# Kernel tuning notes

Measured on AMD Instinct MI355X. Metric: run time of the kernel, lower is better.

## Reference

```python
import jax, jax.numpy as jnp
import numpy as np
import math

T = 2048; HID = 2048; H = 16; KV = 8; G = H // KV; D = 128
GH = 128; BS = 64; NB = T // BS
EPS = 1e-6; RATIO = 0.2; SCALE = 1.0 / math.sqrt(D)


def _rope_tables(length, dim, theta=1000000.0):
    inv = 1.0 / (theta ** (np.arange(0, dim, 2, dtype=np.float32) / dim))
    f = np.outer(np.arange(length, dtype=np.float32), inv)
    emb = np.concatenate([f, f], axis=-1)
    return jnp.asarray(np.cos(emb)), jnp.asarray(np.sin(emb))


def _rot_half(x):
    d = x.shape[-1] // 2
    return jnp.concatenate([-x[..., d:], x[..., :d]], axis=-1)


def _apply_rope(x, cos, sin):
    # x: [T, nH, D], cos/sin: [T, D] broadcast over head dim
    return x * cos[:, None, :] + _rot_half(x) * sin[:, None, :]


def _rmsnorm(x, w, eps=EPS):
    xf = x.astype(jnp.float32)
    v = jnp.mean(xf * xf, axis=-1, keepdims=True)
    return (w * (xf * jax.lax.rsqrt(v + eps))).astype(x.dtype)


def setup_inputs() -> dict:
    key = jax.random.key(0)
    ks = jax.random.split(key, 8)
    s = 0.02
    hidden_states = jax.random.normal(ks[0], (T, HID), jnp.float32)
    Wq = jax.random.normal(ks[1], (HID, H * D), jnp.float32) * s
    Wk = jax.random.normal(ks[2], (HID, KV * D), jnp.float32) * s
    Wv = jax.random.normal(ks[3], (HID, KV * D), jnp.float32) * s
    Wo = jax.random.normal(ks[4], (H * D, HID), jnp.float32) * s
    q_norm_w = jnp.ones((D,), jnp.float32)
    k_norm_w = jnp.ones((D,), jnp.float32)
    gate_wq = jax.random.normal(ks[5], (D, GH), jnp.float32) * s
    gate_wk = jax.random.normal(ks[6], (D, GH), jnp.float32) * s
    cos, sin = _rope_tables(T, D)
    cos_gq, sin_gq = _rope_tables(T, GH)
    cos_blk, sin_blk = _rope_tables(NB, GH)
    # causal block mask: query t may attend to key block j iff j <= t // BS
    block_attention_mask = (jnp.arange(T)[:, None] // BS) >= jnp.arange(NB)[None, :]
    return dict(hidden_states=hidden_states, Wq=Wq, Wk=Wk, Wv=Wv, Wo=Wo,
                q_norm_w=q_norm_w, k_norm_w=k_norm_w, gate_wq=gate_wq, gate_wk=gate_wk,
                cos=cos, sin=sin, cos_gq=cos_gq, sin_gq=sin_gq,
                cos_blk=cos_blk, sin_blk=sin_blk,
                block_attention_mask=block_attention_mask)


def reference(hidden_states, Wq, Wk, Wv, Wo, q_norm_w, k_norm_w, gate_wq, gate_wk,
              cos, sin, cos_gq, sin_gq, cos_blk, sin_blk, block_attention_mask):
    q = (hidden_states @ Wq).reshape(T, H, D)
    k = (hidden_states @ Wk).reshape(T, KV, D)
    v = (hidden_states @ Wv).reshape(T, KV, D)
    q = _rmsnorm(q, q_norm_w)
    k = _rmsnorm(k, k_norm_w)

    # ---- gate network on un-roped q/k: q-head avg-pool to KV heads, k avg-pool per block ----
    q_pool = q.reshape(T, KV, G, D).mean(axis=2)            # [T, KV, D]
    gq = _apply_rope(q_pool @ gate_wq, cos_gq, sin_gq)      # [T, KV, GH]
    k_blk = k.reshape(NB, BS, KV, D).mean(axis=1)           # [NB, KV, D]
    gk = _apply_rope(k_blk @ gate_wk, cos_blk, sin_blk)     # [NB, KV, GH]
    gate_scores = jnp.einsum('tkg,nkg->ktn', gq, gk) / math.sqrt(GH)  # [KV, T, NB]
    predict_mask = jnp.where(block_attention_mask[None], gate_scores, -1e9)

    # ---- main attention (RoPE + GQA causal softmax attention) ----
    qr = _apply_rope(q, cos, sin)
    kr = _apply_rope(k, cos, sin)
    kr_rep = jnp.repeat(kr, G, axis=1)                      # [T, H, D]
    v_rep = jnp.repeat(v, G, axis=1)
    logits = jnp.einsum('thd,shd->hts', qr, kr_rep) * SCALE  # [H, T, T]
    causal = jnp.tril(jnp.ones((T, T), bool))
    logits = jnp.where(causal[None], logits, -jnp.inf)
    probs = jax.nn.softmax(logits, axis=-1)
    attn_output = jnp.einsum('hts,shd->thd', probs, v_rep).reshape(T, H * D) @ Wo

    # ---- pooled ground-truth block mask: attention mass per key block ----
    pooled = probs.reshape(H, T, NB, BS).sum(axis=-1)        # [H, T, NB]
    gt = pooled.reshape(KV, G, T, NB).max(axis=1)            # max_pool3d over head groups -> [KV,T,NB]
    gt = jnp.where(block_attention_mask[None], gt, 0.0)
    gt = gt / (gt.sum(axis=-1, keepdims=True) + 1e-9)

    # ---- KLDiv gate loss on the tail slice (bsz = 1) ----
    start = int(T * RATIO)
    tgt = gt[:, start:, :]                                   # [KV, L, NB]
    logp = jax.nn.log_softmax(predict_mask[:, start:, :], axis=-1)
    safe_t = jnp.where(tgt > 0, tgt, 1.0)
    kl = jnp.where(tgt > 0, tgt * (jnp.log(safe_t) - logp), 0.0)
    gate_loss = kl.reshape(KV, -1).mean(axis=-1).sum()       # KLDivLoss(reduction='mean') per kv head, summed, /bsz(=1)
    return attn_output, gate_loss
```

## Files before the change

kernel.cpp:

```cpp
#include <hip/hip_runtime.h>

#define T_ 2048
#define HID_ 2048
#define H_ 16
#define KV_ 8
#define G_ 2
#define D_ 128
#define GH_ 128
#define BS_ 64
#define NB_ 32
#define START_ 409
#define TG0_ 384
#define SCALE_ 0.08838834764831845f
#define MFIX_ 8.0f

typedef __attribute__((ext_vector_type(8))) short short8_t;
typedef __attribute__((ext_vector_type(4))) float float4_t;
typedef __attribute__((ext_vector_type(8))) unsigned short ushort8_t;
typedef __attribute__((ext_vector_type(4))) unsigned short ushort4_t;

__device__ __forceinline__ float wave_sum(float v) {
#pragma unroll
  for (int o = 32; o > 0; o >>= 1) v += __shfl_xor(v, o, 64);
  return v;
}
__device__ __forceinline__ unsigned short f2bf(float x) {
  unsigned int u = __float_as_uint(x);
  unsigned int r = (u + 0x7fffu + ((u >> 16) & 1u)) >> 16;
  return (unsigned short)r;
}

__device__ __forceinline__ void gload16(const void* g, void* l) {
  __builtin_amdgcn_global_load_lds((const __attribute__((address_space(1))) unsigned int*)g,
                                   (__attribute__((address_space(3))) unsigned int*)l, 16, 0, 0);
}

__device__ __forceinline__ void castT_dev(const float* __restrict__ in,
                                          unsigned short* __restrict__ out, int K, int N,
                                          int ldin, int bx, int by,
                                          unsigned short (*tile)[72], int tid) {
  int k0 = by * 64, n0 = bx * 64;
  int tx = tid & 63, ty4 = tid >> 6;
#pragma unroll
  for (int i = 0; i < 16; ++i) {
    int ky = ty4 * 16 + i;
    tile[tx][ky] = f2bf(in[(size_t)(k0 + ky) * ldin + n0 + tx]);
  }
  __syncthreads();
#pragma unroll
  for (int i = 0; i < 16; ++i) {
    int ny = ty4 * 16 + i;
    out[(size_t)(n0 + ny) * K + k0 + tx] = tile[ny][tx];
  }
}

__global__ __launch_bounds__(256) void prep_cast(const float* __restrict__ hs,
                                                 const float* __restrict__ Wq,
                                                 const float* __restrict__ Wk,
                                                 const float* __restrict__ Wv,
                                                 const float* __restrict__ Wo,
                                                 const float* __restrict__ gwq,
                                                 const float* __restrict__ gwk,
                                                 unsigned short* __restrict__ hsb,
                                                 unsigned short* __restrict__ WqkvT,
                                                 unsigned short* __restrict__ WoT,
                                                 unsigned short* __restrict__ gwqT,
                                                 unsigned short* __restrict__ gwkT) {
  __shared__ unsigned short tile[64][72];
  int id = blockIdx.x, tid = threadIdx.x;
  if (id < 4096) {
    int i = id * 256 + tid;
    float4 v = ((const float4*)hs)[i];
    ushort4_t o = {f2bf(v.x), f2bf(v.y), f2bf(v.z), f2bf(v.w)};
    *(ushort4_t*)(hsb + (size_t)i * 4) = o;
  } else if (id < 5120) {
    int t = id - 4096;
    castT_dev(Wq, WqkvT, 2048, 2048, 2048, t & 31, t >> 5, tile, tid);
  } else if (id < 5632) {
    int t = id - 5120;
    castT_dev(Wk, WqkvT + (size_t)2048 * 2048, 2048, 1024, 1024, t & 15, t >> 4, tile, tid);
  } else if (id < 6144) {
    int t = id - 5632;
    castT_dev(Wv, WqkvT + (size_t)3072 * 2048, 2048, 1024, 1024, t & 15, t >> 4, tile, tid);
  } else if (id < 7168) {
    int t = id - 6144;
    castT_dev(Wo, WoT, 2048, 2048, 2048, t & 31, t >> 5, tile, tid);
  } else if (id < 7172) {
    int t = id - 7168;
    castT_dev(gwq, gwqT, 128, 128, 128, t & 1, t >> 1, tile, tid);
  } else {
    int t = id - 7172;
    castT_dev(gwk, gwkT, 128, 128, 128, t & 1, t >> 1, tile, tid);
  }
}

__device__ __forceinline__ void gemm_body(const unsigned short* __restrict__ A,
                                          const unsigned short* __restrict__ Bt,
                                          float* __restrict__ C,
                                          int M, int N, int K, int ldc, int bx, int by,
                                          unsigned short* As, unsigned short* Bs) {
  int tid = threadIdx.x;
  int wid = tid >> 6, lane = tid & 63;
  int quad = lane >> 4, l16 = lane & 15;
  int wm = wid & 1, wn = wid >> 1;
  int m0 = by * 128, n0 = bx * 128;
  const unsigned short* gA[4];
  const unsigned short* gB[4];
#pragma unroll
  for (int it = 0; it < 4; ++it) {
    int line = wid * 32 + it * 8 + (lane >> 3);
    int chunk = (lane & 7) ^ (line & 7);
    gA[it] = A + (size_t)(m0 + line) * K + chunk * 8;
    gB[it] = Bt + (size_t)(n0 + line) * K + chunk * 8;
  }
  float4_t acc[4][4];
#pragma unroll
  for (int i = 0; i < 4; ++i)
#pragma unroll
    for (int j = 0; j < 4; ++j) acc[i][j] = (float4_t){0.f, 0.f, 0.f, 0.f};
  int nk = K >> 6;
#pragma unroll
  for (int it = 0; it < 4; ++it) {
    gload16(gA[it], As + (wid * 32 + it * 8) * 64);
    gload16(gB[it], Bs + (wid * 32 + it * 8) * 64);
  }
  for (int t = 0; t < nk; ++t) {
    __syncthreads();
    if (t + 1 < nk) {
      int bo = ((t + 1) & 1) * 8192;
#pragma unroll
      for (int it = 0; it < 4; ++it) {
        gload16(gA[it] + (t + 1) * 64, As + bo + (wid * 32 + it * 8) * 64);
        gload16(gB[it] + (t + 1) * 64, Bs + bo + (wid * 32 + it * 8) * 64);
      }
    }
    const unsigned short* Asc = As + (t & 1) * 8192;
    const unsigned short* Bsc = Bs + (t & 1) * 8192;
    short8_t a[2][4], b[2][4];
#pragma unroll
    for (int ks = 0; ks < 2; ++ks) {
      int sw = ((ks * 4 + quad) ^ (l16 & 7)) * 8;
#pragma unroll
      for (int i = 0; i < 4; ++i) {
        a[ks][i] = *(const short8_t*)&Asc[(wm * 64 + i * 16 + l16) * 64 + sw];
        b[ks][i] = *(const short8_t*)&Bsc[(wn * 64 + i * 16 + l16) * 64 + sw];
      }
    }
#pragma unroll
    for (int ks = 0; ks < 2; ++ks)
#pragma unroll
      for (int i = 0; i < 4; ++i)
#pragma unroll
        for (int j = 0; j < 4; ++j)
          acc[i][j] = __builtin_amdgcn_mfma_f32_16x16x32_bf16(a[ks][i], b[ks][j], acc[i][j], 0, 0, 0);
  }
#pragma unroll
  for (int i = 0; i < 4; ++i)
#pragma unroll
    for (int j = 0; j < 4; ++j)
#pragma unroll
      for (int reg = 0; reg < 4; ++reg)
        C[(size_t)(m0 + wm * 64 + i * 16 + quad * 4 + reg) * ldc + n0 + wn * 64 + j * 16 + l16] =
            acc[i][j][reg];
}

__global__ __launch_bounds__(256) void gemm_bf16_v3(const unsigned short* __restrict__ A,
                                                    const unsigned short* __restrict__ Bt,
                                                    float* __restrict__ C,
                                                    int M, int N, int K, int ldc) {
  __shared__ unsigned short As[2 * 128 * 64];
  __shared__ unsigned short Bs[2 * 128 * 64];
  int lin = blockIdx.y * gridDim.x + blockIdx.x;
  int nwg = gridDim.x * gridDim.y;
  int q = nwg >> 3;
  int v = (lin & 7) * q + (lin >> 3);
  int bx = v % gridDim.x, by = v / gridDim.x;
  gemm_body(A, Bt, C, M, N, K, ldc, bx, by, As, Bs);
}

__global__ __launch_bounds__(128) void norm_rope_fused(const float* __restrict__ qkvf,
                                                       const float* __restrict__ qw,
                                                       const float* __restrict__ kw,
                                                       const float* __restrict__ cosT,
                                                       const float* __restrict__ sinT,
                                                       unsigned short* __restrict__ qbf,
                                                       unsigned short* __restrict__ qpool_bf,
                                                       unsigned short* __restrict__ kbf,
                                                       float* __restrict__ knorm) {
  int t = blockIdx.x, d = threadIdx.x;
  int kv = blockIdx.y;
  float cv = cosT[t * D_ + d], sv = sinT[t * D_ + d];
  {
    size_t i0 = (size_t)t * 4096 + (kv * G_) * D_ + d;
    float x0 = qkvf[i0], x1 = qkvf[i0 + D_];
    __shared__ float sred[2][2];
    float s0 = wave_sum(x0 * x0), s1 = wave_sum(x1 * x1);
    if ((d & 63) == 0) { sred[0][d >> 6] = s0; sred[1][d >> 6] = s1; }
    __syncthreads();
    float wv = qw[d];
    float n0 = x0 * rsqrtf((sred[0][0] + sred[0][1]) * (1.f / D_) + 1e-6f) * wv;
    float n1 = x1 * rsqrtf((sred[1][0] + sred[1][1]) * (1.f / D_) + 1e-6f) * wv;
    if (t >= TG0_) qpool_bf[((size_t)(t - TG0_) * KV_ + kv) * D_ + d] = f2bf(0.5f * (n0 + n1));
    __shared__ float sh[2][D_];
    sh[0][d] = n0; sh[1][d] = n1;
    __syncthreads();
    float r0 = (d < 64) ? -sh[0][d + 64] : sh[0][d - 64];
    float r1 = (d < 64) ? -sh[1][d + 64] : sh[1][d - 64];
    qbf[((size_t)(t * H_) + kv * G_) * D_ + d] = f2bf(n0 * cv + r0 * sv);
    qbf[((size_t)(t * H_) + kv * G_ + 1) * D_ + d] = f2bf(n1 * cv + r1 * sv);
  }
  __syncthreads();
  {
    float x = qkvf[(size_t)t * 4096 + 2048 + kv * D_ + d];
    __shared__ float sredk[2];
    float s0 = wave_sum(x * x);
    if ((d & 63) == 0) sredk[d >> 6] = s0;
    __syncthreads();
    float nk = x * rsqrtf((sredk[0] + sredk[1]) * (1.f / D_) + 1e-6f) * kw[d];
    knorm[(size_t)(t * KV_ + kv) * D_ + d] = nk;
    __shared__ float shk[D_];
    shk[d] = nk;
    __syncthreads();
    float rot = (d < 64) ? -shk[d + 64] : shk[d - 64];
    kbf[(size_t)(t * KV_ + kv) * D_ + d] = f2bf(nk * cv + rot * sv);
  }
}

__global__ __launch_bounds__(256) void castT_kblk(const float* __restrict__ qkvf,
                                                  unsigned short* __restrict__ vt,
                                                  const float* __restrict__ knorm,
                                                  unsigned short* __restrict__ kblk_bf) {
  __shared__ unsigned short tile[64][72];
  int id = blockIdx.x, tid = threadIdx.x;
  if (id < 512) {
    castT_dev(qkvf + 3072, vt, T_, 1024, 4096, id & 15, id >> 4, tile, tid);
  } else {
    int task = (id - 512) * 2 + (tid >> 7);
    int n = task >> 3, kv = task & 7, d = tid & 127;
    float s = 0.f;
    for (int i = 0; i < BS_; ++i) s += knorm[((size_t)(n * BS_ + i) * KV_ + kv) * D_ + d];
    kblk_bf[(size_t)(n * KV_ + kv) * D_ + d] = f2bf(s * (1.f / BS_));
  }
}

__global__ __launch_bounds__(128) void rope_g_fused(float* __restrict__ gq, float* __restrict__ gk,
                                                    const float* __restrict__ cosG,
                                                    const float* __restrict__ sinG,
                                                    const float* __restrict__ cosB,
                                                    const float* __restrict__ sinB) {
  int r = blockIdx.x, kvh = blockIdx.y, d = threadIdx.x;
  float* x;
  size_t base;
  float c_, s_;
  if (r < NB_) {
    x = gk;
    base = (size_t)(r * KV_ + kvh) * GH_;
    c_ = cosB[r * GH_ + d]; s_ = sinB[r * GH_ + d];
  } else {
    int rr = r - NB_;
    x = gq;
    base = (size_t)(rr * KV_ + kvh) * GH_;
    c_ = cosG[(size_t)(TG0_ + rr) * GH_ + d]; s_ = sinG[(size_t)(TG0_ + rr) * GH_ + d];
  }
  __shared__ float sh[GH_];
  sh[d] = x[base + d];
  __syncthreads();
  float rot = (d < 64) ? -sh[d + 64] : sh[d - 64];
  x[base + d] = sh[d] * c_ + rot * s_;
}

__global__ __launch_bounds__(256, 2) void attn_gates(const unsigned short* __restrict__ qbf,
                                                     const unsigned short* __restrict__ kbf,
                                                     const unsigned short* __restrict__ vt,
                                                     float* __restrict__ pooled,
                                                     float* __restrict__ o_acc,
                                                     float* __restrict__ l_acc,
                                                     const unsigned short* __restrict__ Aq,
                                                     const unsigned short* __restrict__ Bq,
                                                     float* __restrict__ Cq,
                                                     const unsigned short* __restrict__ Ak,
                                                     const unsigned short* __restrict__ Bk,
                                                     float* __restrict__ Ck) {
  __shared__ unsigned short Ks[2][64 * 128];
  __shared__ unsigned short Vs[2][128 * 64];
  __shared__ unsigned short Ps[8][16 * 64];
  int kv = blockIdx.x;
  int yy = blockIdx.y;
  if (yy >= 64) {
    int g2 = kv + ((yy - 64) << 3);
    unsigned short* As = &Ks[0][0];
    unsigned short* Bs = &Vs[0][0];
    if (g2 < 104)      gemm_body(Aq, Bq, Cq, 13312, 128, 128, 128, 0, g2, As, Bs);
    else if (g2 < 106) gemm_body(Ak, Bk, Ck, 256, 128, 128, 128, 0, g2 - 104, As, Bs);
    return;
  }
  int tile, c_lo, c_hi;
  if (yy < 32) { tile = yy;      c_lo = 0;                c_hi = (tile + 2) >> 1; }
  else         { tile = 63 - yy; c_lo = (tile + 2) >> 1;  c_hi = tile + 1; }
  int t0 = tile * 64;
  int tid = threadIdx.x;
  int wid = tid >> 6, lane = tid & 63;
  int quad = lane >> 4, l16 = lane & 15;

  const unsigned short* kbase[4];
  const unsigned short* vbase[4];
#pragma unroll
  for (int it = 0; it < 4; ++it) {
    int seg = wid * 4 + it;
    int krow = seg * 4 + (lane >> 4);
    int kchk = lane & 15;
    kbase[it] = kbf + ((size_t)krow * KV_ + kv) * D_ + ((kchk ^ (krow & 7)) << 3);
    int vrow = seg * 8 + (lane >> 3);
    int vchk = lane & 7;
    vbase[it] = vt + (size_t)(kv * 128 + vrow) * T_ + ((vchk ^ (vrow & 7)) << 3);
  }

  int tq = t0 + wid * 16 + l16;
  short8_t qf[2][4];
#pragma unroll
  for (int hh = 0; hh < 2; ++hh)
#pragma unroll
    for (int kb = 0; kb < 4; ++kb)
      qf[hh][kb] = *(const short8_t*)&qbf[((size_t)tq * H_ + kv * G_ + hh) * D_ + kb * 32 + quad * 8];

  const short one_bf = (short)0x3F80;
  short8_t ones = {one_bf, one_bf, one_bf, one_bf, one_bf, one_bf, one_bf, one_bf};

  int tbase = t0 + wid * 16 + quad * 4;
  float l_[2][4] = {};
  float pacc[2][2][4] = {};
  float4_t o[2][8];
#pragma unroll
  for (int hh = 0; hh < 2; ++hh)
#pragma unroll
    for (int j = 0; j < 8; ++j) o[hh][j] = (float4_t){0.f, 0.f, 0.f, 0.f};

#pragma unroll
  for (int it = 0; it < 4; ++it) {
    gload16(kbase[it] + (size_t)c_lo * 65536, &Ks[c_lo & 1][(wid * 4 + it) * 512]);
    gload16(vbase[it] + c_lo * 64, &Vs[c_lo & 1][(wid * 4 + it) * 512]);
  }
  for (int c = c_lo; c < c_hi; ++c) {
    __syncthreads();
    if (c + 1 < c_hi) {
      int b = (c + 1) & 1;
#pragma unroll
      for (int it = 0; it < 4; ++it) {
        gload16(kbase[it] + (size_t)(c + 1) * 65536, &Ks[b][(wid * 4 + it) * 512]);
        gload16(vbase[it] + (c + 1) * 64, &Vs[b][(wid * 4 + it) * 512]);
      }
    }
    const unsigned short* Ksc = Ks[c & 1];
    const unsigned short* Vsc = Vs[c & 1];
    int half = c >> 4, cl = c & 15;

    float4_t s[2][4];
#pragma unroll
    for (int j = 0; j < 4; ++j) {
      float4_t a0 = (float4_t){0.f, 0.f, 0.f, 0.f};
      float4_t a1 = (float4_t){0.f, 0.f, 0.f, 0.f};
#pragma unroll
      for (int kb = 0; kb < 4; ++kb) {
        short8_t kf = *(const short8_t*)&Ksc[(j * 16 + l16) * 128 + (((kb * 4 + quad) ^ (l16 & 7)) << 3)];
        a0 = __builtin_amdgcn_mfma_f32_16x16x32_bf16(qf[0][kb], kf, a0, 0, 0, 0);
        a1 = __builtin_amdgcn_mfma_f32_16x16x32_bf16(qf[1][kb], kf, a1, 0, 0, 0);
      }
      s[0][j] = a0;
      s[1][j] = a1;
    }
#pragma unroll
    for (int hh = 0; hh < 2; ++hh) {
      if (c == tile) {
#pragma unroll
        for (int reg = 0; reg < 4; ++reg) {
          int trow = tbase + reg;
#pragma unroll
          for (int j = 0; j < 4; ++j) {
            float p = __expf(s[hh][j][reg] * SCALE_ - MFIX_);
            s[hh][j][reg] = (c * 64 + j * 16 + l16 <= trow) ? p : 0.f;
          }
        }
      } else {
#pragma unroll
        for (int j = 0; j < 4; ++j)
#pragma unroll
          for (int reg = 0; reg < 4; ++reg)
            s[hh][j][reg] = __expf(s[hh][j][reg] * SCALE_ - MFIX_);
      }
#pragma unroll
      for (int j = 0; j < 4; ++j)
#pragma unroll
        for (int reg = 0; reg < 4; ++reg) {
          int r = quad * 4 + reg;
          Ps[wid * 2 + hh][r * 64 + ((j * 16 + l16) ^ ((r & 7) << 3))] = f2bf(s[hh][j][reg]);
        }
    }
    float4_t pool[2] = {(float4_t){0.f, 0.f, 0.f, 0.f}, (float4_t){0.f, 0.f, 0.f, 0.f}};
#pragma unroll
    for (int ks = 0; ks < 2; ++ks) {
      int psw = l16 * 64 + (((ks * 4 + quad) ^ (l16 & 7)) << 3);
      short8_t pf0 = *(const short8_t*)&Ps[wid * 2 + 0][psw];
      short8_t pf1 = *(const short8_t*)&Ps[wid * 2 + 1][psw];
      pool[0] = __builtin_amdgcn_mfma_f32_16x16x32_bf16(pf0, ones, pool[0], 0, 0, 0);
      pool[1] = __builtin_amdgcn_mfma_f32_16x16x32_bf16(pf1, ones, pool[1], 0, 0, 0);
#pragma unroll
      for (int jt = 0; jt < 8; ++jt) {
        short8_t vf = *(const short8_t*)&Vsc[(jt * 16 + l16) * 64 + (((ks * 4 + quad) ^ (l16 & 7)) << 3)];
        o[0][jt] = __builtin_amdgcn_mfma_f32_16x16x32_bf16(pf0, vf, o[0][jt], 0, 0, 0);
        o[1][jt] = __builtin_amdgcn_mfma_f32_16x16x32_bf16(pf1, vf, o[1][jt], 0, 0, 0);
      }
    }
#pragma unroll
    for (int hh = 0; hh < 2; ++hh)
#pragma unroll
      for (int reg = 0; reg < 4; ++reg) {
        l_[hh][reg] += pool[hh][reg];
        if (l16 == cl) pacc[hh][half][reg] = pool[hh][reg];
      }
  }
#pragma unroll
  for (int hh = 0; hh < 2; ++hh) {
    int h = kv * G_ + hh;
#pragma unroll
    for (int reg = 0; reg < 4; ++reg) {
      int trow = tbase + reg;
      if (l16 >= c_lo && l16 < c_hi)
        pooled[((size_t)h * T_ + trow) * NB_ + l16] = pacc[hh][0][reg];
      if (16 + l16 >= c_lo && 16 + l16 < c_hi)
        pooled[((size_t)h * T_ + trow) * NB_ + 16 + l16] = pacc[hh][1][reg];
    }
#pragma unroll
    for (int jt = 0; jt < 8; ++jt)
#pragma unroll
      for (int reg = 0; reg < 4; ++reg)
        atomicAdd(&o_acc[(((size_t)h * T_) + tbase + reg) * D_ + jt * 16 + l16], o[hh][jt][reg]);
    if (l16 == 0) {
#pragma unroll
      for (int reg = 0; reg < 4; ++reg)
        atomicAdd(&l_acc[(size_t)h * T_ + tbase + reg], l_[hh][reg]);
    }
  }
}

__device__ __forceinline__ void gate_loss_body(const float* __restrict__ gq,
                                               const float* __restrict__ gk,
                                               const float* __restrict__ pooled,
                                               const float* __restrict__ l_acc,
                                               float* __restrict__ klsum,
                                               int kv, int yblk, float4* gks4) {
  int tid = threadIdx.x;
#pragma unroll
  for (int p = 0; p < 4; ++p) {
    int f = p * 256 + tid;
    int n = f >> 5, d4 = f & 31;
    gks4[n * 32 + (d4 ^ (n & 7))] =
        *(const float4*)(gk + ((size_t)n * KV_ + kv) * GH_ + d4 * 4);
  }
  __syncthreads();
  int sub = tid >> 5;
  int n = tid & 31;
  int tloc = yblk * 8 + sub;
  bool act = tloc < (T_ - START_);
  int t = START_ + (act ? tloc : 0);
  const float4* a = (const float4*)(gq + ((size_t)(t - TG0_) * KV_ + kv) * GH_);
  float dot = 0.f;
#pragma unroll
  for (int d4 = 0; d4 < 32; ++d4) {
    float4 av = a[d4];
    float4 bv = gks4[n * 32 + (d4 ^ (n & 7))];
    dot += av.x * bv.x + av.y * bv.y + av.z * bv.z + av.w * bv.w;
  }
  bool valid = (t / BS_) >= n;
  float score = valid ? dot * SCALE_ : -1e9f;
  float M = score;
#pragma unroll
  for (int o = 16; o > 0; o >>= 1) M = fmaxf(M, __shfl_xor(M, o, 64));
  float e = __expf(score - M);
  float Z = e;
#pragma unroll
  for (int o = 16; o > 0; o >>= 1) Z += __shfl_xor(Z, o, 64);
  float logZ = M + logf(Z);
  float g = 0.f;
  if (valid) {
    float rl0 = 1.f / l_acc[(size_t)(kv * G_) * T_ + t];
    float rl1 = 1.f / l_acc[(size_t)(kv * G_ + 1) * T_ + t];
    float p0 = pooled[((size_t)(kv * G_) * T_ + t) * NB_ + n] * rl0;
    float p1 = pooled[((size_t)(kv * G_ + 1) * T_ + t) * NB_ + n] * rl1;
    g = fmaxf(p0, p1);
  }
  float gs = g;
#pragma unroll
  for (int o = 16; o > 0; o >>= 1) gs += __shfl_xor(gs, o, 64);
  float tgt = g / (gs + 1e-9f);
  float kl = (tgt > 0.f) ? tgt * (logf(tgt) - (score - logZ)) : 0.f;
  float ks = kl;
#pragma unroll
  for (int o = 16; o > 0; o >>= 1) ks += __shfl_xor(ks, o, 64);
  if (n == 0 && act) klsum[kv * (T_ - START_) + tloc] = ks;
}

__global__ __launch_bounds__(256) void combine_gate(const float* __restrict__ o_acc,
                                                    const float* __restrict__ l_acc,
                                                    unsigned short* __restrict__ attnb,
                                                    const float* __restrict__ gq,
                                                    const float* __restrict__ gk,
                                                    const float* __restrict__ pooled,
                                                    float* __restrict__ klsum) {
  __shared__ float4 gks4[1024];
  int id = blockIdx.x;
  if (id < 1640) {
    gate_loss_body(gq, gk, pooled, l_acc, klsum, id & 7, id >> 3, gks4);
  } else {
    int gid = (id - 1640) * 256 + threadIdx.x;
    int row = gid >> 5, q4 = gid & 31;
    int h = row >> 11, t = row & 2047;
    float inv = 1.f / l_acc[row];
    float4 a = ((const float4*)o_acc)[gid];
    ushort4_t ov = {f2bf(a.x * inv), f2bf(a.y * inv), f2bf(a.z * inv), f2bf(a.w * inv)};
    *(ushort4_t*)(attnb + (size_t)t * (H_ * D_) + h * D_ + q4 * 4) = ov;
  }
}

__global__ __launch_bounds__(256) void wo_gemm_final(const unsigned short* __restrict__ A,
                                                     const unsigned short* __restrict__ Bt,
                                                     float* __restrict__ C,
                                                     const float* __restrict__ klsum,
                                                     float* __restrict__ lout) {
  __shared__ unsigned short As[2 * 128 * 64];
  __shared__ unsigned short Bs[2 * 128 * 64];
  if (blockIdx.y < 16) {
    int lin = blockIdx.y * 16 + blockIdx.x;
    int v = (lin & 7) * 32 + (lin >> 3);
    gemm_body(A, Bt, C, 2048, 2048, 2048, 2048, v & 15, v >> 4, As, Bs);
  } else if (blockIdx.x == 0) {
    const int n = KV_ * (T_ - START_);
    float s = 0.f;
    for (int i = threadIdx.x; i < n; i += 256) s += klsum[i];
    s = wave_sum(s);
    float* sh = (float*)As;
    if ((threadIdx.x & 63) == 0) sh[threadIdx.x >> 6] = s;
    __syncthreads();
    if (threadIdx.x == 0)
      lout[0] = (sh[0] + sh[1] + sh[2] + sh[3]) * (1.f / ((float)(T_ - START_) * NB_));
  }
}

extern "C" void kernel_launch(void* const* d_in, const int* in_sizes, int n_in,
                              void* d_out, int out_size, void* d_ws, size_t ws_size,
                              hipStream_t stream) {
  const float* hs   = (const float*)d_in[0];
  const float* Wq   = (const float*)d_in[1];
  const float* Wk   = (const float*)d_in[2];
  const float* Wv   = (const float*)d_in[3];
  const float* Wo   = (const float*)d_in[4];
  const float* qw   = (const float*)d_in[5];
  const float* kw   = (const float*)d_in[6];
  const float* gwq  = (const float*)d_in[7];
  const float* gwk  = (const float*)d_in[8];
  const float* cosT = (const float*)d_in[9];
  const float* sinT = (const float*)d_in[10];
  const float* cosG = (const float*)d_in[11];
  const float* sinG = (const float*)d_in[12];
  const float* cosB = (const float*)d_in[13];
  const float* sinB = (const float*)d_in[14];
  float* out = (float*)d_out;
  float* ws = (float*)d_ws;
  const size_t MEG = 1048576;

  float*          qkvf     = ws;
  unsigned short* attnb    = (unsigned short*)ws;
  float*          pooled   = ws + 2 * MEG;
  float*          klsum    = ws + 3 * MEG;
  float*          l_acc    = ws + 3 * MEG + 65536;
  float*          o_acc    = ws + 4 * MEG;
  unsigned short* WqkvT    = (unsigned short*)(ws + 8 * MEG);
  unsigned short* qbf      = WqkvT;
  unsigned short* kbf      = WqkvT + 4 * MEG;
  unsigned short* vt       = WqkvT + 6 * MEG;
  unsigned short* hsb      = (unsigned short*)(ws + 12 * MEG);
  float*          knorm    = ws + 12 * MEG;
  unsigned short* WoT      = (unsigned short*)(ws + 14 * MEG);
  unsigned short* qpool_bf = (unsigned short*)(ws + 16 * MEG);
  float*          gq       = ws + 17 * MEG;
  unsigned short* kblk_bf  = (unsigned short*)(ws + 18 * MEG + 786432);
  float*          gk       = ws + 18 * MEG + 819200;
  unsigned short* gwqT     = (unsigned short*)(ws + 18 * MEG + 851968);
  unsigned short* gwkT     = (unsigned short*)(ws + 18 * MEG + 860160);

  prep_cast<<<7176, 256, 0, stream>>>(hs, Wq, Wk, Wv, Wo, gwq, gwk, hsb, WqkvT, WoT, gwqT, gwkT);
  gemm_bf16_v3<<<dim3(32, 16), 256, 0, stream>>>(hsb, WqkvT, qkvf, 2048, 4096, 2048, 4096);
  norm_rope_fused<<<dim3(T_, 8), 128, 0, stream>>>(qkvf, qw, kw, cosT, sinT, qbf, qpool_bf,
                                                   kbf, knorm);
  castT_kblk<<<640, 256, 0, stream>>>(qkvf, vt, knorm, kblk_bf);
  hipMemsetAsync(o_acc, 0, (size_t)4 * MEG * sizeof(float), stream);
  hipMemsetAsync(l_acc, 0, (size_t)H_ * T_ * sizeof(float), stream);
  attn_gates<<<dim3(KV_, 78), 256, 0, stream>>>(qbf, kbf, vt, pooled, o_acc, l_acc,
                                                qpool_bf, gwqT, gq, kblk_bf, gwkT, gk);
  rope_g_fused<<<dim3(NB_ + (T_ - TG0_), KV_), 128, 0, stream>>>(gq, gk, cosG, sinG, cosB, sinB);
  combine_gate<<<1640 + 4096, 256, 0, stream>>>(o_acc, l_acc, attnb, gq, gk, pooled, klsum);
  wo_gemm_final<<<dim3(16, 17), 256, 0, stream>>>(attnb, WoT, out, klsum, out + (size_t)T_ * HID_);
  finalize_loss:;
}
```

Before: 303.9 us.

## Fuse gate RoPE into gate GEMM epilogue, split-K Wo GEMM, fold memsets into kernel

The gate-projection GEMMs in attn_gates now apply the rotary embedding in their epilogue, using an LDS round-trip to fetch the rotated half, which removes the separate rope_g_fused launch. The Wo GEMM is split along K into two halves that accumulate into the output with atomicAdd, doubling the workgroup count so more CUs are busy. The memsets for o_acc, l_acc and the output are folded into the castT_kblk launch as extra zeroing blocks. In exchange, fp32 atomic accumulation makes the output order-dependent and adds atomic traffic, and the output must be zeroed beforehand.

```diff
diff --git a/kernel.cpp b/kernel.cpp
--- a/kernel.cpp
+++ b/kernel.cpp
@@ -94,26 +94,24 @@
   }
 }
 
-__device__ __forceinline__ void gemm_body(const unsigned short* __restrict__ A,
+__device__ __forceinline__ void gemm_core(const unsigned short* __restrict__ A,
                                           const unsigned short* __restrict__ Bt,
-                                          float* __restrict__ C,
-                                          int M, int N, int K, int ldc, int bx, int by,
-                                          unsigned short* As, unsigned short* Bs) {
+                                          int K, int lda, int ldb, int m0, int n0,
+                                          unsigned short* As, unsigned short* Bs,
+                                          float4_t (&acc)[4][4]) {
   int tid = threadIdx.x;
   int wid = tid >> 6, lane = tid & 63;
   int quad = lane >> 4, l16 = lane & 15;
   int wm = wid & 1, wn = wid >> 1;
-  int m0 = by * 128, n0 = bx * 128;
   const unsigned short* gA[4];
   const unsigned short* gB[4];
 #pragma unroll
   for (int it = 0; it < 4; ++it) {
     int line = wid * 32 + it * 8 + (lane >> 3);
     int chunk = (lane & 7) ^ (line & 7);
-    gA[it] = A + (size_t)(m0 + line) * K + chunk * 8;
-    gB[it] = Bt + (size_t)(n0 + line) * K + chunk * 8;
-  }
-  float4_t acc[4][4];
+    gA[it] = A + (size_t)(m0 + line) * lda + chunk * 8;
+    gB[it] = Bt + (size_t)(n0 + line) * ldb + chunk * 8;
+  }
 #pragma unroll
   for (int i = 0; i < 4; ++i)
 #pragma unroll
@@ -154,6 +152,14 @@
         for (int j = 0; j < 4; ++j)
           acc[i][j] = __builtin_amdgcn_mfma_f32_16x16x32_bf16(a[ks][i], b[ks][j], acc[i][j], 0, 0, 0);
   }
+}
+
+__device__ __forceinline__ void gemm_store(float* __restrict__ C, int ldc, int m0, int n0,
+                                           float4_t (&acc)[4][4]) {
+  int tid = threadIdx.x;
+  int wid = tid >> 6, lane = tid & 63;
+  int quad = lane >> 4, l16 = lane & 15;
+  int wm = wid & 1, wn = wid >> 1;
 #pragma unroll
   for (int i = 0; i < 4; ++i)
 #pragma unroll
@@ -162,20 +168,38 @@
       for (int reg = 0; reg < 4; ++reg)
         C[(size_t)(m0 + wm * 64 + i * 16 + quad * 4 + reg) * ldc + n0 + wn * 64 + j * 16 + l16] =
             acc[i][j][reg];
+}
+
+__device__ __forceinline__ void gemm_atomic(float* __restrict__ C, int ldc, int m0, int n0,
+                                            float4_t (&acc)[4][4]) {
+  int tid = threadIdx.x;
+  int wid = tid >> 6, lane = tid & 63;
+  int quad = lane >> 4, l16 = lane & 15;
+  int wm = wid & 1, wn = wid >> 1;
+#pragma unroll
+  for (int i = 0; i < 4; ++i)
+#pragma unroll
+    for (int j = 0; j < 4; ++j)
+#pragma unroll
+      for (int reg = 0; reg < 4; ++reg)
+        atomicAdd(&C[(size_t)(m0 + wm * 64 + i * 16 + quad * 4 + reg) * ldc + n0 + wn * 64 + j * 16 + l16],
+                  acc[i][j][reg]);
 }
 
 __global__ __launch_bounds__(256) void gemm_bf16_v3(const unsigned short* __restrict__ A,
                                                     const unsigned short* __restrict__ Bt,
                                                     float* __restrict__ C,
                                                     int M, int N, int K, int ldc) {
-  __shared__ unsigned short As[2 * 128 * 64];
-  __shared__ unsigned short Bs[2 * 128 * 64];
+  __shared__ unsigned short As[2 * 8192];
+  __shared__ unsigned short Bs[2 * 8192];
   int lin = blockIdx.y * gridDim.x + blockIdx.x;
   int nwg = gridDim.x * gridDim.y;
   int q = nwg >> 3;
   int v = (lin & 7) * q + (lin >> 3);
   int bx = v % gridDim.x, by = v / gridDim.x;
-  gemm_body(A, Bt, C, M, N, K, ldc, bx, by, As, Bs);
+  float4_t acc[4][4];
+  gemm_core(A, Bt, K, K, K, by * 128, bx * 128, As, Bs, acc);
+  gemm_store(C, ldc, by * 128, bx * 128, acc);
 }
 
 __global__ __launch_bounds__(128) void norm_rope_fused(const float* __restrict__ qkvf,
@@ -229,44 +253,34 @@
 __global__ __launch_bounds__(256) void castT_kblk(const float* __restrict__ qkvf,
                                                   unsigned short* __restrict__ vt,
                                                   const float* __restrict__ knorm,
-                                                  unsigned short* __restrict__ kblk_bf) {
+                                                  unsigned short* __restrict__ kblk_bf,
+                                                  float* __restrict__ o_acc,
+                                                  float* __restrict__ outz,
+                                                  float* __restrict__ l_acc) {
   __shared__ unsigned short tile[64][72];
   int id = blockIdx.x, tid = threadIdx.x;
+  const float4 z = {0.f, 0.f, 0.f, 0.f};
   if (id < 512) {
     castT_dev(qkvf + 3072, vt, T_, 1024, 4096, id & 15, id >> 4, tile, tid);
-  } else {
+  } else if (id < 640) {
     int task = (id - 512) * 2 + (tid >> 7);
     int n = task >> 3, kv = task & 7, d = tid & 127;
     float s = 0.f;
     for (int i = 0; i < BS_; ++i) s += knorm[((size_t)(n * BS_ + i) * KV_ + kv) * D_ + d];
     kblk_bf[(size_t)(n * KV_ + kv) * D_ + d] = f2bf(s * (1.f / BS_));
-  }
-}
-
-__global__ __launch_bounds__(128) void rope_g_fused(float* __restrict__ gq, float* __restrict__ gk,
-                                                    const float* __restrict__ cosG,
-                                                    const float* __restrict__ sinG,
-                                                    const float* __restrict__ cosB,
-                                                    const float* __restrict__ sinB) {
-  int r = blockIdx.x, kvh = blockIdx.y, d = threadIdx.x;
-  float* x;
-  size_t base;
-  float c_, s_;
-  if (r < NB_) {
-    x = gk;
-    base = (size_t)(r * KV_ + kvh) * GH_;
-    c_ = cosB[r * GH_ + d]; s_ = sinB[r * GH_ + d];
+  } else if (id < 1664) {
+    float4* p = (float4*)o_acc + (size_t)(id - 640) * 1024;
+#pragma unroll
+    for (int k = 0; k < 4; ++k) p[k * 256 + tid] = z;
+  } else if (id < 2688) {
+    float4* p = (float4*)outz + (size_t)(id - 1664) * 1024;
+#pragma unroll
+    for (int k = 0; k < 4; ++k) p[k * 256 + tid] = z;
   } else {
-    int rr = r - NB_;
-    x = gq;
-    base = (size_t)(rr * KV_ + kvh) * GH_;
-    c_ = cosG[(size_t)(TG0_ + rr) * GH_ + d]; s_ = sinG[(size_t)(TG0_ + rr) * GH_ + d];
-  }
-  __shared__ float sh[GH_];
-  sh[d] = x[base + d];
-  __syncthreads();
-  float rot = (d < 64) ? -sh[d + 64] : sh[d - 64];
-  x[base + d] = sh[d] * c_ + rot * s_;
+    float4* p = (float4*)l_acc;
+#pragma unroll
+    for (int k = 0; k < 32; ++k) p[k * 256 + tid] = z;
+  }
 }
 
 __global__ __launch_bounds__(256, 2) void attn_gates(const unsigned short* __restrict__ qbf,
@@ -280,27 +294,70 @@
                                                      float* __restrict__ Cq,
                                                      const unsigned short* __restrict__ Ak,
                                                      const unsigned short* __restrict__ Bk,
-                                                     float* __restrict__ Ck) {
-  __shared__ unsigned short Ks[2][64 * 128];
-  __shared__ unsigned short Vs[2][128 * 64];
-  __shared__ unsigned short Ps[8][16 * 64];
+                                                     float* __restrict__ Ck,
+                                                     const float* __restrict__ cosG,
+                                                     const float* __restrict__ sinG,
+                                                     const float* __restrict__ cosB,
+                                                     const float* __restrict__ sinB) {
+  __shared__ __align__(16) unsigned short smem[40960];
+  unsigned short (*Ks)[8192] = (unsigned short(*)[8192])smem;
+  unsigned short (*Vs)[8192] = (unsigned short(*)[8192])(smem + 16384);
+  unsigned short (*Ps)[1024] = (unsigned short(*)[1024])(smem + 32768);
   int kv = blockIdx.x;
   int yy = blockIdx.y;
+  int tid = threadIdx.x;
+  int wid = tid >> 6, lane = tid & 63;
+  int quad = lane >> 4, l16 = lane & 15;
   if (yy >= 64) {
     int g2 = kv + ((yy - 64) << 3);
-    unsigned short* As = &Ks[0][0];
-    unsigned short* Bs = &Vs[0][0];
-    if (g2 < 104)      gemm_body(Aq, Bq, Cq, 13312, 128, 128, 128, 0, g2, As, Bs);
-    else if (g2 < 106) gemm_body(Ak, Bk, Ck, 256, 128, 128, 128, 0, g2 - 104, As, Bs);
+    if (g2 >= 106) return;
+    bool isQ = g2 < 104;
+    const unsigned short* Ag = isQ ? Aq : Ak;
+    const unsigned short* Bg = isQ ? Bq : Bk;
+    float* Cg = isQ ? Cq : Ck;
+    int by = isQ ? g2 : g2 - 104;
+    float4_t acc[4][4];
+    gemm_core(Ag, Bg, 128, 128, 128, by * 128, 0, smem, smem + 16384, acc);
+    int wm = wid & 1, wn = wid >> 1;
+    __syncthreads();
+    float* lf = (float*)smem;
+#pragma unroll
+    for (int i = 0; i < 4; ++i)
+#pragma unroll
+      for (int j = 0; j < 4; ++j)
+#pragma unroll
+        for (int reg = 0; reg < 4; ++reg)
+          lf[(wm * 64 + i * 16 + quad * 4 + reg) * 128 + wn * 64 + j * 16 + l16] = acc[i][j][reg];
+    __syncthreads();
+#pragma unroll
+    for (int i = 0; i < 4; ++i)
+#pragma unroll
+      for (int j = 0; j < 4; ++j)
+#pragma unroll
+        for (int reg = 0; reg < 4; ++reg) {
+          int rl = wm * 64 + i * 16 + quad * 4 + reg;
+          int col = wn * 64 + j * 16 + l16;
+          float v = acc[i][j][reg];
+          float prt = lf[rl * 128 + (col ^ 64)];
+          float rot = (col < 64) ? -prt : prt;
+          int grow = by * 128 + rl;
+          int rr = grow >> 3;
+          float cv, sv;
+          if (isQ) {
+            cv = cosG[(size_t)(TG0_ + rr) * GH_ + col];
+            sv = sinG[(size_t)(TG0_ + rr) * GH_ + col];
+          } else {
+            cv = cosB[rr * GH_ + col];
+            sv = sinB[rr * GH_ + col];
+          }
+          Cg[(size_t)grow * GH_ + col] = v * cv + rot * sv;
+        }
     return;
   }
   int tile, c_lo, c_hi;
   if (yy < 32) { tile = yy;      c_lo = 0;                c_hi = (tile + 2) >> 1; }
   else         { tile = 63 - yy; c_lo = (tile + 2) >> 1;  c_hi = tile + 1; }
   int t0 = tile * 64;
-  int tid = threadIdx.x;
-  int wid = tid >> 6, lane = tid & 63;
-  int quad = lane >> 4, l16 = lane & 15;
 
   const unsigned short* kbase[4];
   const unsigned short* vbase[4];
@@ -526,12 +583,15 @@
                                                      float* __restrict__ C,
                                                      const float* __restrict__ klsum,
                                                      float* __restrict__ lout) {
-  __shared__ unsigned short As[2 * 128 * 64];
-  __shared__ unsigned short Bs[2 * 128 * 64];
-  if (blockIdx.y < 16) {
+  __shared__ unsigned short As[2 * 8192];
+  __shared__ unsigned short Bs[2 * 8192];
+  if (blockIdx.y < 32) {
     int lin = blockIdx.y * 16 + blockIdx.x;
-    int v = (lin & 7) * 32 + (lin >> 3);
-    gemm_body(A, Bt, C, 2048, 2048, 2048, 2048, v & 15, v >> 4, As, Bs);
+    int v = (lin & 7) * 64 + (lin >> 3);
+    int bx = v & 15, by = (v >> 4) & 15, kh = v >> 8;
+    float4_t acc[4][4];
+    gemm_core(A + kh * 1024, Bt + kh * 1024, 1024, 2048, 2048, by * 128, bx * 128, As, Bs, acc);
+    gemm_atomic(C, 2048, by * 128, bx * 128, acc);
   } else if (blockIdx.x == 0) {
     const int n = KV_ * (T_ - START_);
     float s = 0.f;
@@ -591,13 +651,10 @@
   gemm_bf16_v3<<<dim3(32, 16), 256, 0, stream>>>(hsb, WqkvT, qkvf, 2048, 4096, 2048, 4096);
   norm_rope_fused<<<dim3(T_, 8), 128, 0, stream>>>(qkvf, qw, kw, cosT, sinT, qbf, qpool_bf,
                                                    kbf, knorm);
-  castT_kblk<<<640, 256, 0, stream>>>(qkvf, vt, knorm, kblk_bf);
-  hipMemsetAsync(o_acc, 0, (size_t)4 * MEG * sizeof(float), stream);
-  hipMemsetAsync(l_acc, 0, (size_t)H_ * T_ * sizeof(float), stream);
+  castT_kblk<<<2689, 256, 0, stream>>>(qkvf, vt, knorm, kblk_bf, o_acc, out, l_acc);
   attn_gates<<<dim3(KV_, 78), 256, 0, stream>>>(qbf, kbf, vt, pooled, o_acc, l_acc,
-                                                qpool_bf, gwqT, gq, kblk_bf, gwkT, gk);
-  rope_g_fused<<<dim3(NB_ + (T_ - TG0_), KV_), 128, 0, stream>>>(gq, gk, cosG, sinG, cosB, sinB);
+                                                qpool_bf, gwqT, gq, kblk_bf, gwkT, gk,
+                                                cosG, sinG, cosB, sinB);
   combine_gate<<<1640 + 4096, 256, 0, stream>>>(o_acc, l_acc, attnb, gq, gk, pooled, klsum);
-  wo_gemm_final<<<dim3(16, 17), 256, 0, stream>>>(attnb, WoT, out, klsum, out + (size_t)T_ * HID_);
-  finalize_loss:;
-}
+  wo_gemm_final<<<dim3(16, 33), 256, 0, stream>>>(attnb, WoT, out, klsum, out + (size_t)T_ * HID_);
+}
```

Measured after the change: 313.7 us. 1.03x slower.
